# Kernel optimization log

Measured on AMD Instinct MI355X. Metric: run time of the kernel, lower is better.

Reference implementation:

```python
import jax, jax.numpy as jnp
import numpy as np

D_MODEL = 1024
N_HEADS = 16
D_FF = 4096
EPS = 1e-5


def setup_inputs() -> dict:
    key = jax.random.key(0)
    ks = jax.random.split(key, 16)
    B, S, D, F = 2, 2048, D_MODEL, D_FF
    s_d = 1.0 / np.sqrt(D)
    s_f = 1.0 / np.sqrt(F)
    return {
        "x": jax.random.normal(ks[0], (B, S, D), dtype=jnp.float32),
        "pad_mask": jnp.ones((B, S), dtype=jnp.int32),
        "ln1_g": jnp.ones((D,), jnp.float32), "ln1_b": jnp.zeros((D,), jnp.float32),
        "ln2_g": jnp.ones((D,), jnp.float32), "ln2_b": jnp.zeros((D,), jnp.float32),
        # weights stored [in, out] (equivalent to torch Linear weight.T)
        "wq": jax.random.normal(ks[1], (D, D), jnp.float32) * s_d,
        "bq": jnp.zeros((D,), jnp.float32),
        "wk": jax.random.normal(ks[2], (D, D), jnp.float32) * s_d,
        "bk": jnp.zeros((D,), jnp.float32),
        "wv": jax.random.normal(ks[3], (D, D), jnp.float32) * s_d,
        "bv": jnp.zeros((D,), jnp.float32),
        "wo": jax.random.normal(ks[4], (D, D), jnp.float32) * s_d,
        "bo": jnp.zeros((D,), jnp.float32),
        "w1": jax.random.normal(ks[5], (D, F), jnp.float32) * s_d,
        "b1": jnp.zeros((F,), jnp.float32),
        "w2": jax.random.normal(ks[6], (F, D), jnp.float32) * s_f,
        "b2": jnp.zeros((D,), jnp.float32),
    }


def _layernorm(x, g, b):
    mu = jnp.mean(x, axis=-1, keepdims=True)
    var = jnp.mean(jnp.square(x - mu), axis=-1, keepdims=True)
    return (x - mu) * jax.lax.rsqrt(var + EPS) * g + b


def reference(x, pad_mask, ln1_g, ln1_b, ln2_g, ln2_b,
              wq, bq, wk, bk, wv, bv, wo, bo, w1, b1, w2, b2):
    B, S, D = x.shape
    H = N_HEADS
    dk = D // H

    # mask: causal [1,1,S,S] * pad [B,1,1,S]
    causal = jnp.tril(jnp.ones((S, S), dtype=jnp.int32))[None, None]
    mask = pad_mask[:, None, None, :] * causal  # [B,1,S,S]

    h = _layernorm(x, ln1_g, ln1_b)
    q = (h @ wq + bq).reshape(B, S, H, dk).transpose(0, 2, 1, 3)
    k = (h @ wk + bk).reshape(B, S, H, dk).transpose(0, 2, 1, 3)
    v = (h @ wv + bv).reshape(B, S, H, dk).transpose(0, 2, 1, 3)

    scores = jnp.einsum('bhqd,bhkd->bhqk', q, k) / np.sqrt(dk)
    scores = jnp.where(mask == 0, -jnp.inf, scores)
    attn = jax.nn.softmax(scores, axis=-1)
    ctx = jnp.einsum('bhqk,bhkd->bhqd', attn, v)
    ctx = ctx.transpose(0, 2, 1, 3).reshape(B, S, D)
    x = x + ctx @ wo + bo

    h2 = _layernorm(x, ln2_g, ln2_b)
    ff = jax.nn.gelu(h2 @ w1 + b1, approximate=False) @ w2 + b2
    return x + ff
```

## Files before the change

kernel.cpp:

```cpp
#include <hip/hip_runtime.h>
#include <math.h>


typedef unsigned short bfu;
typedef unsigned short u16x4 __attribute__((ext_vector_type(4)));
typedef unsigned short u16x8 __attribute__((ext_vector_type(8)));
typedef __bf16         bf16x8 __attribute__((ext_vector_type(8)));
typedef float          f32x4 __attribute__((ext_vector_type(4)));

#define SEQ   2048
#define NTOK  4096
#define DM    1024
#define DKH   64

static __device__ __forceinline__ float bfu2f(bfu u) {
  return __uint_as_float(((unsigned)u) << 16);
}
static __device__ __forceinline__ bfu f2bfu(float f) {
  unsigned u = __float_as_uint(f);
  u += 0x7FFFu + ((u >> 16) & 1u);
  return (bfu)(u >> 16);
}
static __device__ __forceinline__ float ldF(const void* p, size_t i, bool isbf) {
  return isbf ? bfu2f(((const bfu*)p)[i]) : ((const float*)p)[i];
}
static __device__ __forceinline__ bool dt_isbf(const void* dt) {
  return *(const unsigned*)dt == 0x3F803F80u;
}
static __device__ __forceinline__ void g2l16(const void* g, void* l) {
  __builtin_amdgcn_global_load_lds((const __attribute__((address_space(1))) void*)g,
                                   (__attribute__((address_space(3))) void*)l,
                                   16, 0, 0);
}

static __device__ __forceinline__ void tr_tile(const void* in, bfu* out,
                                               int R, int C, int gx, int gy,
                                               bool isbf, bfu t[64][65]) {
  const int tx = threadIdx.x & 63, ty = threadIdx.x >> 6;
#pragma unroll
  for (int i = 0; i < 16; ++i) {
    int rr = i * 4 + ty;
    size_t idx = (size_t)(gy + rr) * C + gx + tx;
    t[rr][tx] = isbf ? ((const bfu*)in)[idx] : f2bfu(((const float*)in)[idx]);
  }
  __syncthreads();
#pragma unroll
  for (int i = 0; i < 16; ++i) {
    int cc = i * 4 + ty;
    out[(size_t)(gx + cc) * R + gy + tx] = t[tx][cc];
  }
}

__global__ __launch_bounds__(256) void prep_k(
    const void* ln1g, const void* ln1b, const void* ln2g, const void* ln2b,
    const void* bq, const void* bk, const void* bv, const void* bo,
    const void* b1, const void* b2,
    const void* wq, const void* wk, const void* wv, const void* wo,
    const void* w1, const void* w2,
    bfu* __restrict__ vecs, bfu* __restrict__ wqkvT, bfu* __restrict__ woT,
    bfu* __restrict__ w1T, bfu* __restrict__ w2T) {
  __shared__ bfu t[64][65];
  const bool isbf = dt_isbf(ln1g);
  const int bid = blockIdx.x, tid = threadIdx.x;
  if (bid < 52) {
    const void* src; int segStart, segDst;
    if      (bid < 4)  { src = ln1g; segStart = 0;  segDst = 0; }
    else if (bid < 8)  { src = ln1b; segStart = 4;  segDst = 1024; }
    else if (bid < 12) { src = ln2g; segStart = 8;  segDst = 2048; }
    else if (bid < 16) { src = ln2b; segStart = 12; segDst = 3072; }
    else if (bid < 20) { src = bq;   segStart = 16; segDst = 4096; }
    else if (bid < 24) { src = bk;   segStart = 20; segDst = 5120; }
    else if (bid < 28) { src = bv;   segStart = 24; segDst = 6144; }
    else if (bid < 32) { src = bo;   segStart = 28; segDst = 7168; }
    else if (bid < 48) { src = b1;   segStart = 32; segDst = 8192; }
    else               { src = b2;   segStart = 48; segDst = 12288; }
    const int off = (bid - segStart) * 256 + tid;
    vecs[segDst + off] = isbf ? ((const bfu*)src)[off]
                              : f2bfu(((const float*)src)[off]);
    return;
  }
  const void* in; bfu* out; int R, C, gx, gy;
  const int j = bid - 52;
  if (j < 1024) {
    const int mat = j >> 8, rem = j & 255;
    in  = (mat == 0) ? wq : (mat == 1) ? wk : (mat == 2) ? wv : wo;
    out = (mat == 0) ? wqkvT : (mat == 1) ? wqkvT + 1048576
        : (mat == 2) ? wqkvT + 2097152 : woT;
    R = 1024; C = 1024; gx = (rem & 15) * 64; gy = (rem >> 4) * 64;
  } else if (j < 2048) {
    const int rem = j - 1024;
    in = w1; out = w1T; R = 1024; C = 4096;
    gx = (rem & 63) * 64; gy = (rem >> 6) * 64;
  } else {
    const int rem = j - 2048;
    in = w2; out = w2T; R = 4096; C = 1024;
    gx = (rem & 15) * 64; gy = (rem >> 4) * 64;
  }
  tr_tile(in, out, R, C, gx, gy, isbf, t);
}

__global__ __launch_bounds__(256) void trw2_k(const void* __restrict__ w2,
                                              bfu* __restrict__ out,
                                              const void* __restrict__ dt) {
  __shared__ bfu t[64][65];
  const bool isbf = dt_isbf(dt);
  const int rem = blockIdx.x;
  tr_tile(w2, out, 4096, 1024, (rem & 15) * 64, (rem >> 4) * 64, isbf, t);
}

template <bool RAW>
__global__ __launch_bounds__(256) void ln_k(const void* __restrict__ xin,
                                            const bfu* __restrict__ g,
                                            const bfu* __restrict__ bb,
                                            bfu* __restrict__ y,
                                            const void* __restrict__ dt) {
  const int t = threadIdx.x;
  const size_t base = (size_t)blockIdx.x * DM;
  const int c0 = t * 4;
  float v[4];
  bool isbf = true;
  if constexpr (RAW) isbf = dt_isbf(dt);
  if (!RAW || isbf) {
    u16x4 u = *(const u16x4*)((const bfu*)xin + base + c0);
#pragma unroll
    for (int i = 0; i < 4; ++i) v[i] = bfu2f(u[i]);
  } else {
    float4 f = *(const float4*)((const float*)xin + base + c0);
    v[0] = f.x; v[1] = f.y; v[2] = f.z; v[3] = f.w;
  }
  float s1 = v[0] + v[1] + v[2] + v[3];
  float s2 = v[0]*v[0] + v[1]*v[1] + v[2]*v[2] + v[3]*v[3];
#pragma unroll
  for (int o = 32; o; o >>= 1) {
    s1 += __shfl_xor(s1, o);
    s2 += __shfl_xor(s2, o);
  }
  __shared__ float r1[4], r2[4];
  const int wid = t >> 6, lane = t & 63;
  if (lane == 0) { r1[wid] = s1; r2[wid] = s2; }
  __syncthreads();
  s1 = r1[0] + r1[1] + r1[2] + r1[3];
  s2 = r2[0] + r2[1] + r2[2] + r2[3];
  const float mu = s1 * (1.0f / DM);
  const float var = s2 * (1.0f / DM) - mu * mu;
  const float rs = rsqrtf(var + 1e-5f);
  u16x4 gv = *(const u16x4*)&g[c0];
  u16x4 bv = *(const u16x4*)&bb[c0];
  u16x4 ov;
#pragma unroll
  for (int i = 0; i < 4; ++i)
    ov[i] = f2bfu((v[i] - mu) * rs * bfu2f(gv[i]) + bfu2f(bv[i]));
  *(u16x4*)&y[base + c0] = ov;
}

template <int EPI>
__global__ __launch_bounds__(256) void gemm_bt(const bfu* __restrict__ A,
                                               const bfu* __restrict__ Bt,
                                               const bfu* __restrict__ bias,
                                               const void* __restrict__ res,
                                               void* __restrict__ C,
                                               int M, int N, int K,
                                               const void* __restrict__ dt) {
  __shared__ __align__(16) bfu Asm[128 * 32];
  __shared__ __align__(16) bfu Bsm[128 * 32];
  const bool isbf = dt_isbf(dt);
  const int tid = threadIdx.x;
  const int m0 = blockIdx.y * 128, n0 = blockIdx.x * 128;
  const int wid = tid >> 6, lane = tid & 63;
  const int wm = (wid >> 1) * 64, wn = (wid & 1) * 64;
  const int quad = lane >> 4, l16 = lane & 15;

  f32x4 acc[4][4] = {};

  const int c0 = tid, c1 = tid + 256;
  const bfu* agp0 = A + (size_t)(m0 + (c0 >> 2)) * K + (c0 & 3) * 8;
  const bfu* agp1 = A + (size_t)(m0 + (c1 >> 2)) * K + (c1 & 3) * 8;
  const bfu* bgp0 = Bt + (size_t)(n0 + (c0 >> 2)) * K + (c0 & 3) * 8;
  const bfu* bgp1 = Bt + (size_t)(n0 + (c1 >> 2)) * K + (c1 & 3) * 8;
  bfu* al0 = Asm + c0 * 8;
  bfu* al1 = Asm + c1 * 8;
  bfu* bl0 = Bsm + c0 * 8;
  bfu* bl1 = Bsm + c1 * 8;

  for (int k0 = 0; k0 < K; k0 += 32) {
    g2l16(agp0 + k0, al0);
    g2l16(agp1 + k0, al1);
    g2l16(bgp0 + k0, bl0);
    g2l16(bgp1 + k0, bl1);
    __syncthreads();

    u16x8 af[4], bfr[4];
#pragma unroll
    for (int i = 0; i < 4; ++i)
      af[i] = *(const u16x8*)&Asm[(wm + i * 16 + l16) * 32 + quad * 8];
#pragma unroll
    for (int i = 0; i < 4; ++i)
      bfr[i] = *(const u16x8*)&Bsm[(wn + i * 16 + l16) * 32 + quad * 8];
#pragma unroll
    for (int mi = 0; mi < 4; ++mi)
#pragma unroll
      for (int ni = 0; ni < 4; ++ni)
        acc[mi][ni] = __builtin_amdgcn_mfma_f32_16x16x32_bf16(
            __builtin_bit_cast(bf16x8, af[mi]),
            __builtin_bit_cast(bf16x8, bfr[ni]), acc[mi][ni], 0, 0, 0);
    __syncthreads();
  }

#pragma unroll
  for (int mi = 0; mi < 4; ++mi) {
#pragma unroll
    for (int ni = 0; ni < 4; ++ni) {
      const int col = n0 + wn + ni * 16 + l16;
      const float bvv = bfu2f(bias[col]);
#pragma unroll
      for (int r = 0; r < 4; ++r) {
        const int row = m0 + wm + mi * 16 + quad * 4 + r;
        const size_t idx = (size_t)row * N + col;
        float v = acc[mi][ni][r] + bvv;
        if constexpr (EPI == 1) {
          v = 0.5f * v * (1.0f + erff(v * 0.70710678118f));
          ((bfu*)C)[idx] = f2bfu(v);
        } else if constexpr (EPI == 2) {
          v += ldF(res, idx, isbf);
          ((bfu*)C)[idx] = f2bfu(v);
        } else if constexpr (EPI == 3) {
          v += bfu2f(((const bfu*)res)[idx]);
          if (isbf) ((bfu*)C)[idx] = f2bfu(v);
          else      ((float*)C)[idx] = v;
        } else {
          ((bfu*)C)[idx] = f2bfu(v);
        }
      }
    }
  }
}

template <int EPI>
__global__ __launch_bounds__(256) void gemm32_bt(const bfu* __restrict__ A,
                                                 const bfu* __restrict__ Bt,
                                                 const bfu* __restrict__ bias,
                                                 const void* __restrict__ res,
                                                 void* __restrict__ C,
                                                 int M, int N, int K,
                                                 const void* __restrict__ dt) {
  __shared__ __align__(16) bfu Asm[2 * 32 * 32];
  __shared__ __align__(16) bfu Bsm[2 * 128 * 32];
  const bool isbf = dt_isbf(dt);
  const int tid = threadIdx.x;
  const int m0 = blockIdx.y * 32, n0 = blockIdx.x * 128;
  const int wid = tid >> 6, lane = tid & 63;
  const int wn = wid * 32;
  const int quad = lane >> 4, l16 = lane & 15;

  f32x4 acc[2][2] = {};

  const int pA = tid >> 7, rA = (tid >> 2) & 31, qA = tid & 3;
  const bfu* agp = A + (size_t)(m0 + rA) * K + pA * 32 + qA * 8;
  bfu* aldst = Asm + tid * 8;
  const bfu* bgp[4]; bfu* bldst[4];
#pragma unroll
  for (int s = 0; s < 4; ++s) {
    const int c = tid + s * 256;
    const int pB = c >> 9, rB = (c >> 2) & 127, qB = c & 3;
    bgp[s] = Bt + (size_t)(n0 + rB) * K + pB * 32 + qB * 8;
    bldst[s] = Bsm + c * 8;
  }

  for (int k0 = 0; k0 < K; k0 += 64) {
    g2l16(agp + k0, aldst);
#pragma unroll
    for (int s = 0; s < 4; ++s) g2l16(bgp[s] + k0, bldst[s]);
    __syncthreads();

    u16x8 af[2][2], bfr[2][2];
#pragma unroll
    for (int kt = 0; kt < 2; ++kt) {
#pragma unroll
      for (int mi = 0; mi < 2; ++mi)
        af[mi][kt] = *(const u16x8*)&Asm[kt * 1024 + (mi * 16 + l16) * 32 + quad * 8];
#pragma unroll
      for (int ni = 0; ni < 2; ++ni)
        bfr[ni][kt] = *(const u16x8*)&Bsm[kt * 4096 + (wn + ni * 16 + l16) * 32 + quad * 8];
    }
#pragma unroll
    for (int kt = 0; kt < 2; ++kt)
#pragma unroll
      for (int mi = 0; mi < 2; ++mi)
#pragma unroll
        for (int ni = 0; ni < 2; ++ni)
          acc[mi][ni] = __builtin_amdgcn_mfma_f32_16x16x32_bf16(
              __builtin_bit_cast(bf16x8, af[mi][kt]),
              __builtin_bit_cast(bf16x8, bfr[ni][kt]), acc[mi][ni], 0, 0, 0);
    __syncthreads();
  }

#pragma unroll
  for (int mi = 0; mi < 2; ++mi) {
#pragma unroll
    for (int ni = 0; ni < 2; ++ni) {
      const int col = n0 + wn + ni * 16 + l16;
      const float bvv = bfu2f(bias[col]);
#pragma unroll
      for (int r = 0; r < 4; ++r) {
        const int row = m0 + mi * 16 + quad * 4 + r;
        const size_t idx = (size_t)row * N + col;
        float v = acc[mi][ni][r] + bvv;
        if constexpr (EPI == 1) {
          v = 0.5f * v * (1.0f + erff(v * 0.70710678118f));
          ((bfu*)C)[idx] = f2bfu(v);
        } else if constexpr (EPI == 2) {
          v += ldF(res, idx, isbf);
          ((bfu*)C)[idx] = f2bfu(v);
        } else if constexpr (EPI == 3) {
          v += bfu2f(((const bfu*)res)[idx]);
          if (isbf) ((bfu*)C)[idx] = f2bfu(v);
          else      ((float*)C)[idx] = v;
        } else {
          ((bfu*)C)[idx] = f2bfu(v);
        }
      }
    }
  }
}

#define NEG_BIG (-1e30f)
#define KSTR 72

__global__ __launch_bounds__(256) void attn_flash(const bfu* __restrict__ qkv,
                                                  const int* __restrict__ pad,
                                                  bfu* __restrict__ ctx) {
  __shared__ __align__(16) bfu Kb[64 * KSTR];
  __shared__ __align__(16) bfu VT[64 * KSTR];
  __shared__ __align__(16) bfu Pb[4][16 * KSTR];

  const int tid = threadIdx.x;
  const int wid = tid >> 6, lane = tid & 63;
  const int quad = lane >> 4, l16 = lane & 15;
  const int bh = blockIdx.x;
  const int b = bh >> 4, h = bh & 15;
  const int yq = blockIdx.y;
  const int qt = (yq < 8) ? yq : (yq < 16) ? 23 - yq
               : (yq < 24) ? yq : 55 - yq;
  const int q0 = qt * 64;

  const bfu* qptr = qkv + (size_t)(b * SEQ + q0 + wid * 16 + l16) * 3072 + h * 64 + quad * 8;
  u16x8 qfr[2];
#pragma unroll
  for (int kt = 0; kt < 2; ++kt) {
    u16x8 qr = *(const u16x8*)(qptr + kt * 32);
#pragma unroll
    for (int j = 0; j < 8; ++j) qr[j] = f2bfu(bfu2f(qr[j]) * 0.125f);
    qfr[kt] = qr;
  }

  f32x4 Ofr[4] = {};
  float mrow[4], lrow[4];
#pragma unroll
  for (int r = 0; r < 4; ++r) { mrow[r] = NEG_BIG; lrow[r] = 0.0f; }

  const bfu* kvbase = qkv + (size_t)(b * SEQ) * 3072 + h * 64;
  const int* pb = pad + b * SEQ;
  const int qrow_base = q0 + wid * 16 + quad * 4;

  const int kkey0 = tid >> 3,          kpc0 = tid & 7;
  const int kkey1 = (tid + 256) >> 3,  kpc1 = (tid + 256) & 7;
  const int vkey = tid & 63, dblk = tid >> 6;

  u16x8 kreg0, kreg1, vreg0, vreg1;
  kreg0 = *(const u16x8*)(kvbase + (size_t)kkey0 * 3072 + 1024 + kpc0 * 8);
  kreg1 = *(const u16x8*)(kvbase + (size_t)kkey1 * 3072 + 1024 + kpc1 * 8);
  vreg0 = *(const u16x8*)(kvbase + (size_t)vkey * 3072 + 2048 + dblk * 16);
  vreg1 = *(const u16x8*)(kvbase + (size_t)vkey * 3072 + 2048 + dblk * 16 + 8);

  const int ntiles = qt + 1;
  for (int t = 0; t < ntiles; ++t) {
    const int k0 = t * 64;
    __syncthreads();

    *(u16x8*)&Kb[kkey0 * KSTR + kpc0 * 8] = kreg0;
    *(u16x8*)&Kb[kkey1 * KSTR + kpc1 * 8] = kreg1;
#pragma unroll
    for (int j = 0; j < 8; ++j) VT[(dblk * 16 + j) * KSTR + vkey] = vreg0[j];
#pragma unroll
    for (int j = 0; j < 8; ++j) VT[(dblk * 16 + 8 + j) * KSTR + vkey] = vreg1[j];
    __syncthreads();

    if (t + 1 < ntiles) {
      const int kn = k0 + 64;
      kreg0 = *(const u16x8*)(kvbase + (size_t)(kn + kkey0) * 3072 + 1024 + kpc0 * 8);
      kreg1 = *(const u16x8*)(kvbase + (size_t)(kn + kkey1) * 3072 + 1024 + kpc1 * 8);
      vreg0 = *(const u16x8*)(kvbase + (size_t)(kn + vkey) * 3072 + 2048 + dblk * 16);
      vreg1 = *(const u16x8*)(kvbase + (size_t)(kn + vkey) * 3072 + 2048 + dblk * 16 + 8);
    }

    f32x4 S[4] = {};
#pragma unroll
    for (int nt = 0; nt < 4; ++nt)
#pragma unroll
      for (int kt = 0; kt < 2; ++kt) {
        u16x8 bf = *(const u16x8*)&Kb[(nt * 16 + l16) * KSTR + kt * 32 + quad * 8];
        S[nt] = __builtin_amdgcn_mfma_f32_16x16x32_bf16(
            __builtin_bit_cast(bf16x8, qfr[kt]),
            __builtin_bit_cast(bf16x8, bf), S[nt], 0, 0, 0);
      }

    const bool edge = (t == qt);
    float p[4][4];
    float cmax[4] = {NEG_BIG, NEG_BIG, NEG_BIG, NEG_BIG};
#pragma unroll
    for (int nt = 0; nt < 4; ++nt) {
      const int key = k0 + nt * 16 + l16;
      const bool ok = (pb[key] != 0);
#pragma unroll
      for (int r = 0; r < 4; ++r) {
        float s = (ok && (!edge || key <= qrow_base + r)) ? S[nt][r] : NEG_BIG;
        p[nt][r] = s;
        cmax[r] = fmaxf(cmax[r], s);
      }
    }
#pragma unroll
    for (int off = 1; off < 16; off <<= 1)
#pragma unroll
      for (int r = 0; r < 4; ++r)
        cmax[r] = fmaxf(cmax[r], __shfl_xor(cmax[r], off));
    float alpha[4];
#pragma unroll
    for (int r = 0; r < 4; ++r) {
      const float mn = fmaxf(mrow[r], cmax[r]);
      alpha[r] = __expf(mrow[r] - mn);
      mrow[r] = mn;
    }
    float psum[4] = {0, 0, 0, 0};
#pragma unroll
    for (int nt = 0; nt < 4; ++nt)
#pragma unroll
      for (int r = 0; r < 4; ++r) {
        p[nt][r] = __expf(p[nt][r] - mrow[r]);
        psum[r] += p[nt][r];
      }
#pragma unroll
    for (int off = 1; off < 16; off <<= 1)
#pragma unroll
      for (int r = 0; r < 4; ++r) psum[r] += __shfl_xor(psum[r], off);
#pragma unroll
    for (int r = 0; r < 4; ++r) lrow[r] = lrow[r] * alpha[r] + psum[r];
#pragma unroll
    for (int n = 0; n < 4; ++n)
#pragma unroll
      for (int r = 0; r < 4; ++r) Ofr[n][r] *= alpha[r];

#pragma unroll
    for (int nt = 0; nt < 4; ++nt)
#pragma unroll
      for (int r = 0; r < 4; ++r)
        Pb[wid][(quad * 4 + r) * KSTR + nt * 16 + l16] = f2bfu(p[nt][r]);

#pragma unroll
    for (int at = 0; at < 2; ++at) {
      u16x8 af = *(const u16x8*)&Pb[wid][l16 * KSTR + at * 32 + quad * 8];
#pragma unroll
      for (int n = 0; n < 4; ++n) {
        u16x8 bf = *(const u16x8*)&VT[(n * 16 + l16) * KSTR + at * 32 + quad * 8];
        Ofr[n] = __builtin_amdgcn_mfma_f32_16x16x32_bf16(
            __builtin_bit_cast(bf16x8, af),
            __builtin_bit_cast(bf16x8, bf), Ofr[n], 0, 0, 0);
      }
    }
  }

  float inv[4];
#pragma unroll
  for (int r = 0; r < 4; ++r) inv[r] = 1.0f / lrow[r];
#pragma unroll
  for (int n = 0; n < 4; ++n)
#pragma unroll
    for (int r = 0; r < 4; ++r)
      ctx[(size_t)(b * SEQ + qrow_base + r) * DM + h * 64 + n * 16 + l16] =
          f2bfu(Ofr[n][r] * inv[r]);
}

extern "C" void kernel_launch(void* const* d_in, const int* in_sizes, int n_in,
                              void* d_out, int out_size, void* d_ws, size_t ws_size,
                              hipStream_t stream) {
  (void)in_sizes; (void)n_in; (void)out_size;
  const void* x    = d_in[0];
  const int*  pad  = (const int*)d_in[1];
  const void* ln1g = d_in[2];
  const void* ln1b = d_in[3];
  const void* ln2g = d_in[4];
  const void* ln2b = d_in[5];
  const void* wq   = d_in[6];
  const void* bq   = d_in[7];
  const void* wk   = d_in[8];
  const void* bk   = d_in[9];
  const void* wv   = d_in[10];
  const void* bv   = d_in[11];
  const void* wo   = d_in[12];
  const void* bo   = d_in[13];
  const void* w1   = d_in[14];
  const void* b1   = d_in[15];
  const void* w2   = d_in[16];
  const void* b2   = d_in[17];

  const bool flat = ws_size >= (size_t)(37765120 + 1024) * 2;
  bfu* base  = (bfu*)d_ws;
  bfu* vecs  = base;
  bfu* wqkvT = vecs  + 16384;
  bfu* woT   = wqkvT + 3145728;
  bfu* w1T   = woT   + 1048576;
  bfu* w2Tf  = w1T   + 4194304;
  bfu* h     = w2Tf  + (flat ? 4194304 : 0);
  bfu* qkv   = h     + 4194304;
  bfu* ctx   = qkv   + 12582912;
  bfu* x1    = ctx   + 4194304;
  bfu* ffh   = qkv;
  bfu* w2T   = flat ? w2Tf : h;

  const dim3 blk(256);
  bfu* lg1 = vecs;        bfu* lb1 = vecs + 1024;
  bfu* lg2 = vecs + 2048; bfu* lb2 = vecs + 3072;
  bfu* bqkv = vecs + 4096;
  bfu* boc  = vecs + 7168;
  bfu* b1c  = vecs + 8192;
  bfu* b2c  = vecs + 12288;

  prep_k<<<dim3(flat ? 3124 : 2100), blk, 0, stream>>>(
      ln1g, ln1b, ln2g, ln2b, bq, bk, bv, bo, b1, b2,
      wq, wk, wv, wo, w1, w2, vecs, wqkvT, woT, w1T, w2T);

  ln_k<true><<<dim3(NTOK), blk, 0, stream>>>(x, lg1, lb1, h, ln1g);
  gemm_bt<0><<<dim3(24, 32), blk, 0, stream>>>(h, wqkvT, bqkv, nullptr,
                                               qkv, NTOK, 3072, 1024, ln1g);
  attn_flash<<<dim3(32, 32), blk, 0, stream>>>(qkv, pad, ctx);
  gemm32_bt<2><<<dim3(8, 128), blk, 0, stream>>>(ctx, woT, boc, x, x1,
                                                 NTOK, 1024, 1024, ln1g);
  ln_k<false><<<dim3(NTOK), blk, 0, stream>>>(x1, lg2, lb2, h, ln1g);
  gemm_bt<1><<<dim3(32, 32), blk, 0, stream>>>(h, w1T, b1c, nullptr, ffh,
                                               NTOK, 4096, 1024, ln1g);
  if (!flat) trw2_k<<<dim3(1024), blk, 0, stream>>>(w2, w2T, ln1g);
  gemm32_bt<3><<<dim3(8, 128), blk, 0, stream>>>(ffh, w2T, b2c, x1, d_out,
                                                 NTOK, 1024, 4096, ln1g);
}
```

Measured before the change: 451.7 us.

## Replace 128x128 GEMM with 256x256 tile, 4-stage LDS pipeline and swizzle

The QKV and FFN1 GEMMs move from a 128x128 single-buffered tile with 256 threads to a 256x256 tile with 512 threads. The new kernel keeps a 4-deep ring of shared-memory buffers filled by async global-to-LDS loads, paced with vmcnt waits and one barrier per k-step. It also applies an XOR swizzle on the k-chunk to cut LDS bank conflicts and raises wave priority around the MFMA block. This targets load latency and the redundant global traffic of small tiles, at the cost of far fewer blocks (192 and 256, close to the CU count) and higher register and LDS pressure.

Measured after the change: 444.6 us. About the same (-1.6%).

```diff
diff --git a/kernel.cpp b/kernel.cpp
--- a/kernel.cpp
+++ b/kernel.cpp
@@ -154,60 +154,81 @@
 }
 
 template <int EPI>
-__global__ __launch_bounds__(256) void gemm_bt(const bfu* __restrict__ A,
-                                               const bfu* __restrict__ Bt,
-                                               const bfu* __restrict__ bias,
-                                               const void* __restrict__ res,
-                                               void* __restrict__ C,
-                                               int M, int N, int K,
-                                               const void* __restrict__ dt) {
-  __shared__ __align__(16) bfu Asm[128 * 32];
-  __shared__ __align__(16) bfu Bsm[128 * 32];
-  const bool isbf = dt_isbf(dt);
+__global__ __launch_bounds__(512, 2) void gemm256_bt(
+    const bfu* __restrict__ A, const bfu* __restrict__ Bt,
+    const bfu* __restrict__ bias, void* __restrict__ C,
+    int M, int N, int K) {
+  __shared__ __align__(16) bfu sm[4][2][256 * 32];
   const int tid = threadIdx.x;
-  const int m0 = blockIdx.y * 128, n0 = blockIdx.x * 128;
+  const int m0 = blockIdx.y * 256, n0 = blockIdx.x * 256;
   const int wid = tid >> 6, lane = tid & 63;
-  const int wm = (wid >> 1) * 64, wn = (wid & 1) * 64;
   const int quad = lane >> 4, l16 = lane & 15;
-
-  f32x4 acc[4][4] = {};
-
-  const int c0 = tid, c1 = tid + 256;
-  const bfu* agp0 = A + (size_t)(m0 + (c0 >> 2)) * K + (c0 & 3) * 8;
-  const bfu* agp1 = A + (size_t)(m0 + (c1 >> 2)) * K + (c1 & 3) * 8;
-  const bfu* bgp0 = Bt + (size_t)(n0 + (c0 >> 2)) * K + (c0 & 3) * 8;
-  const bfu* bgp1 = Bt + (size_t)(n0 + (c1 >> 2)) * K + (c1 & 3) * 8;
-  bfu* al0 = Asm + c0 * 8;
-  bfu* al1 = Asm + c1 * 8;
-  bfu* bl0 = Bsm + c0 * 8;
-  bfu* bl1 = Bsm + c1 * 8;
-
-  for (int k0 = 0; k0 < K; k0 += 32) {
-    g2l16(agp0 + k0, al0);
-    g2l16(agp1 + k0, al1);
-    g2l16(bgp0 + k0, bl0);
-    g2l16(bgp1 + k0, bl1);
-    __syncthreads();
-
-    u16x8 af[4], bfr[4];
-#pragma unroll
-    for (int i = 0; i < 4; ++i)
-      af[i] = *(const u16x8*)&Asm[(wm + i * 16 + l16) * 32 + quad * 8];
-#pragma unroll
-    for (int i = 0; i < 4; ++i)
-      bfr[i] = *(const u16x8*)&Bsm[(wn + i * 16 + l16) * 32 + quad * 8];
-#pragma unroll
-    for (int mi = 0; mi < 4; ++mi)
+  const int wm = (wid >> 2) * 128, wn = (wid & 3) * 64;
+
+  f32x4 acc[8][4] = {};
+
+  const int c0 = tid, c1 = tid + 512;
+  const int p0 = (c0 & 3) ^ ((c0 >> 3) & 3);
+  const int p1 = (c1 & 3) ^ ((c1 >> 3) & 3);
+  const bfu* aS0 = A  + (size_t)(m0 + (c0 >> 2)) * K + p0 * 8;
+  const bfu* aS1 = A  + (size_t)(m0 + (c1 >> 2)) * K + p1 * 8;
+  const bfu* bS0 = Bt + (size_t)(n0 + (c0 >> 2)) * K + p0 * 8;
+  const bfu* bS1 = Bt + (size_t)(n0 + (c1 >> 2)) * K + p1 * 8;
+
+  const int nt = K >> 5;
+
+#pragma unroll
+  for (int p = 0; p < 3; ++p) {
+    bfu* as = sm[p][0]; bfu* bs = sm[p][1];
+    const int ko = p * 32;
+    g2l16(aS0 + ko, as + c0 * 8);
+    g2l16(aS1 + ko, as + c1 * 8);
+    g2l16(bS0 + ko, bs + c0 * 8);
+    g2l16(bS1 + ko, bs + c1 * 8);
+  }
+  asm volatile("s_waitcnt vmcnt(8)" ::: "memory");
+  __builtin_amdgcn_s_barrier();
+
+  const int ksw = (quad ^ ((l16 >> 1) & 3)) * 8;
+
+  for (int t = 0; t < nt; ++t) {
+    {
+      int ts = t + 3; if (ts >= nt) ts = nt - 1;
+      bfu* as = sm[(t + 3) & 3][0]; bfu* bs = sm[(t + 3) & 3][1];
+      const int ko = ts * 32;
+      g2l16(aS0 + ko, as + c0 * 8);
+      g2l16(aS1 + ko, as + c1 * 8);
+      g2l16(bS0 + ko, bs + c0 * 8);
+      g2l16(bS1 + ko, bs + c1 * 8);
+    }
+    __builtin_amdgcn_sched_barrier(0);
+
+    const bfu* as = sm[t & 3][0]; const bfu* bs = sm[t & 3][1];
+    u16x8 af[8], bfr[4];
+#pragma unroll
+    for (int mi = 0; mi < 8; ++mi)
+      af[mi] = *(const u16x8*)&as[(wm + mi * 16 + l16) * 32 + ksw];
+#pragma unroll
+    for (int ni = 0; ni < 4; ++ni)
+      bfr[ni] = *(const u16x8*)&bs[(wn + ni * 16 + l16) * 32 + ksw];
+
+    __builtin_amdgcn_s_setprio(1);
+#pragma unroll
+    for (int mi = 0; mi < 8; ++mi)
 #pragma unroll
       for (int ni = 0; ni < 4; ++ni)
         acc[mi][ni] = __builtin_amdgcn_mfma_f32_16x16x32_bf16(
             __builtin_bit_cast(bf16x8, af[mi]),
             __builtin_bit_cast(bf16x8, bfr[ni]), acc[mi][ni], 0, 0, 0);
-    __syncthreads();
-  }
-
-#pragma unroll
-  for (int mi = 0; mi < 4; ++mi) {
+    __builtin_amdgcn_s_setprio(0);
+
+    asm volatile("s_waitcnt vmcnt(8)" ::: "memory");
+    __builtin_amdgcn_s_barrier();
+  }
+  asm volatile("s_waitcnt vmcnt(0)" ::: "memory");
+
+#pragma unroll
+  for (int mi = 0; mi < 8; ++mi) {
 #pragma unroll
     for (int ni = 0; ni < 4; ++ni) {
       const int col = n0 + wn + ni * 16 + l16;
@@ -217,19 +238,9 @@
         const int row = m0 + wm + mi * 16 + quad * 4 + r;
         const size_t idx = (size_t)row * N + col;
         float v = acc[mi][ni][r] + bvv;
-        if constexpr (EPI == 1) {
+        if constexpr (EPI == 1)
           v = 0.5f * v * (1.0f + erff(v * 0.70710678118f));
-          ((bfu*)C)[idx] = f2bfu(v);
-        } else if constexpr (EPI == 2) {
-          v += ldF(res, idx, isbf);
-          ((bfu*)C)[idx] = f2bfu(v);
-        } else if constexpr (EPI == 3) {
-          v += bfu2f(((const bfu*)res)[idx]);
-          if (isbf) ((bfu*)C)[idx] = f2bfu(v);
-          else      ((float*)C)[idx] = v;
-        } else {
-          ((bfu*)C)[idx] = f2bfu(v);
-        }
+        ((bfu*)C)[idx] = f2bfu(v);
       }
     }
   }
@@ -529,14 +540,14 @@
       wq, wk, wv, wo, w1, w2, vecs, wqkvT, woT, w1T, w2T);
 
   ln_k<true><<<dim3(NTOK), blk, 0, stream>>>(x, lg1, lb1, h, ln1g);
-  gemm_bt<0><<<dim3(24, 32), blk, 0, stream>>>(h, wqkvT, bqkv, nullptr,
-                                               qkv, NTOK, 3072, 1024, ln1g);
+  gemm256_bt<0><<<dim3(12, 16), dim3(512), 0, stream>>>(h, wqkvT, bqkv, qkv,
+                                                        NTOK, 3072, 1024);
   attn_flash<<<dim3(32, 32), blk, 0, stream>>>(qkv, pad, ctx);
   gemm32_bt<2><<<dim3(8, 128), blk, 0, stream>>>(ctx, woT, boc, x, x1,
                                                  NTOK, 1024, 1024, ln1g);
   ln_k<false><<<dim3(NTOK), blk, 0, stream>>>(x1, lg2, lb2, h, ln1g);
-  gemm_bt<1><<<dim3(32, 32), blk, 0, stream>>>(h, w1T, b1c, nullptr, ffh,
-                                               NTOK, 4096, 1024, ln1g);
+  gemm256_bt<1><<<dim3(16, 16), dim3(512), 0, stream>>>(h, w1T, b1c, ffh,
+                                                        NTOK, 4096, 1024);
   if (!flat) trw2_k<<<dim3(1024), blk, 0, stream>>>(w2, w2T, ln1g);
   gemm32_bt<3><<<dim3(8, 128), blk, 0, stream>>>(ffh, w2T, b2c, x1, d_out,
                                                  NTOK, 1024, 4096, ln1g);
```
